# Kernel tuning notes

Hardware: AMD Instinct MI355X
Metric: run time of the kernel (lower is better)

The kernel has to match this reference:

```python
import jax, jax.numpy as jnp
import numpy as np

N, T, F_IN, E, H, FW = 4096, 64, 8, 256, 512, 32
LN_EPS = 1e-5


def setup_inputs() -> dict:
    key = jax.random.key(0)
    ks = jax.random.split(key, 16)
    nrm = lambda k, s, sc=0.05: jax.random.normal(k, s, dtype=jnp.float32) * sc
    return {
        "x": nrm(ks[0], (N, T, F_IN), 1.0),
        "We": nrm(ks[1], (E, F_IN)), "be": nrm(ks[2], (E,)),
        "Wih0": nrm(ks[3], (4 * H, E)), "Whh0": nrm(ks[4], (4 * H, H)),
        "bih0": nrm(ks[5], (4 * H,)), "bhh0": nrm(ks[6], (4 * H,)),
        "Wih1": nrm(ks[7], (4 * H, H)), "Whh1": nrm(ks[8], (4 * H, H)),
        "bih1": nrm(ks[9], (4 * H,)), "bhh1": nrm(ks[10], (4 * H,)),
        "fc1_w": nrm(ks[11], (H, H)), "fc1_b": nrm(ks[12], (H,)),
        "ln_g": jnp.ones((H,), jnp.float32), "ln_b": jnp.zeros((H,), jnp.float32),
        "fc2_w": nrm(ks[13], (F_IN, H)), "fc2_b": nrm(ks[14], (F_IN,)),
    }


def _cell(x, h, c, Wih, Whh, bih, bhh):
    # PyTorch LSTM gate order: i, f, g, o
    g = x @ Wih.T + h @ Whh.T + (bih + bhh)
    i, f, gg, o = jnp.split(g, 4, axis=-1)
    c = jax.nn.sigmoid(f) * c + jax.nn.sigmoid(i) * jnp.tanh(gg)
    h = jax.nn.sigmoid(o) * jnp.tanh(c)
    return h, c


def _layer(xs, Wih, Whh, bih, bhh):
    # xs: (T, N, D) -> ys: (T, N, H), final (h, c)
    n = xs.shape[1]
    Hd = Whh.shape[1]
    h0 = jnp.zeros((n, Hd), xs.dtype)
    def step(carry, x_t):
        h, c = carry
        h, c = _cell(x_t, h, c, Wih, Whh, bih, bhh)
        return (h, c), h
    (h, c), ys = jax.lax.scan(step, (h0, h0), xs)
    return ys, h, c


def reference(x, We, be, Wih0, Whh0, bih0, bhh0, Wih1, Whh1, bih1, bhh1,
              fc1_w, fc1_b, ln_g, ln_b, fc2_w, fc2_b):
    x_enc = x[:, :-1, :]          # (N, T-1, F)
    x0 = x[:, -1, :]              # (N, F)

    # ---- encoder ----
    emb = x_enc @ We.T + be       # (N, T-1, E)
    xs = jnp.swapaxes(emb, 0, 1)  # (T-1, N, E)
    ys0, h0e, c0e = _layer(xs, Wih0, Whh0, bih0, bhh0)
    _, h1e, c1e = _layer(ys0, Wih1, Whh1, bih1, bhh1)

    # ---- decoder head: Linear -> LayerNorm -> ReLU -> Linear ----
    def fc(h):
        z = h @ fc1_w.T + fc1_b
        mu = z.mean(-1, keepdims=True)
        var = z.var(-1, keepdims=True)
        z = (z - mu) * jax.lax.rsqrt(var + LN_EPS) * ln_g + ln_b
        z = jax.nn.relu(z)
        return z @ fc2_w.T + fc2_b

    def dec_step(carry, _):
        xt, h0, c0, h1, c1 = carry
        e = xt @ We.T + be
        h0, c0 = _cell(e, h0, c0, Wih0, Whh0, bih0, bhh0)
        h1, c1 = _cell(h0, h1, c1, Wih1, Whh1, bih1, bhh1)
        y = fc(h1)
        return (y, h0, c0, h1, c1), y

    _, ys = jax.lax.scan(dec_step, (x0, h0e, c0e, h1e, c1e), None, length=FW)
    return jnp.swapaxes(ys, 0, 1)  # (N, FW, F)
```

## Files before the change

### kernel.cpp

```cpp
#include <hip/hip_runtime.h>
#include <math.h>

#define NB   4096
#define HID  512
#define G4H  2048
#define EDIM 256
#define FINP 8
#define TSTEPS 64
#define FWIN 32

typedef __bf16 bf16;
typedef bf16  bf16x8 __attribute__((ext_vector_type(8)));
typedef float f32x4  __attribute__((ext_vector_type(4)));

__device__ __forceinline__ float sigf(float x) { return 1.0f / (1.0f + __expf(-x)); }
__device__ __forceinline__ float tanhf_(float x) { return 2.0f * sigf(2.0f * x) - 1.0f; }

__device__ __forceinline__ void gload16(const void* g, void* l) {
    __builtin_amdgcn_global_load_lds((const __attribute__((address_space(1))) void*)g,
                                     (__attribute__((address_space(3))) void*)l, 16, 0, 0);
}

__device__ __forceinline__ void gemm_pass(
    const bf16* __restrict__ A, int lda,
    const bf16* __restrict__ W, int ldw,
    int m0, int n0,
    bf16* As, bf16* Ws,
    f32x4 (&acc)[4][4])
{
    const int tid  = threadIdx.x;
    const int lane = tid & 63;
    const int w    = tid >> 6;
    const int wr   = w >> 1, wc = w & 1;
    const int koct = lane >> 4;
    const int l16  = lane & 15;

    const int lin0 = tid;
    const int lin1 = tid + 256;
    const int ar0 = lin0 >> 2, ac0 = (lin0 & 3) * 8;
    const int ar1 = lin1 >> 2, ac1 = (lin1 & 3) * 8;

    for (int k0 = 0; k0 < HID; k0 += 32) {
        __syncthreads();
        gload16(A + (size_t)(m0 + ar0) * lda + k0 + ac0, As + lin0 * 8);
        gload16(A + (size_t)(m0 + ar1) * lda + k0 + ac1, As + lin1 * 8);
        gload16(W + (size_t)(n0 + ar0) * ldw + k0 + ac0, Ws + lin0 * 8);
        gload16(W + (size_t)(n0 + ar1) * ldw + k0 + ac1, Ws + lin1 * 8);
        __syncthreads();
        bf16x8 af[4], bfr[4];
#pragma unroll
        for (int m = 0; m < 4; ++m)
            af[m] = *(const bf16x8*)&As[(wr * 64 + m * 16 + l16) * 32 + koct * 8];
#pragma unroll
        for (int n = 0; n < 4; ++n)
            bfr[n] = *(const bf16x8*)&Ws[(wc * 64 + n * 16 + l16) * 32 + koct * 8];
#pragma unroll
        for (int m = 0; m < 4; ++m)
#pragma unroll
            for (int n = 0; n < 4; ++n)
                acc[m][n] = __builtin_amdgcn_mfma_f32_16x16x32_bf16(af[m], bfr[n], acc[m][n], 0, 0, 0);
    }
}

template<int NPASS, bool HASX>
__global__ __launch_bounds__(256)
void lstm_mfma(const bf16* __restrict__ A1, const bf16* __restrict__ W1,
               const bf16* __restrict__ A2, const bf16* __restrict__ W2,
               const float* __restrict__ Wfc, const float* __restrict__ bias,
               const float* __restrict__ xA, int sx,
               float* __restrict__ cst, bf16* __restrict__ hdst)
{
    __shared__ bf16 As[128 * 32];
    __shared__ bf16 Ws[128 * 32];
    f32x4 acc[4][4];
#pragma unroll
    for (int m = 0; m < 4; ++m)
#pragma unroll
        for (int n = 0; n < 4; ++n)
            acc[m][n] = (f32x4){0.f, 0.f, 0.f, 0.f};

    const int m0 = blockIdx.x * 128, n0 = blockIdx.y * 128;
    gemm_pass(A1, 1024, W1, 512, m0, n0, As, Ws, acc);
    if constexpr (NPASS == 2)
        gemm_pass(A2, 1024, W2, 512, m0, n0, As, Ws, acc);

    const int tid = threadIdx.x, lane = tid & 63, w = tid >> 6;
    const int wr = w >> 1, wc = w & 1, l16 = lane & 15, lq = lane >> 4;
    const int hu = blockIdx.y * 32 + wc * 16 + l16;
    const int jb = n0 + wc * 64 + l16;

    float bq[4];
    float wf[4][8];
#pragma unroll
    for (int g = 0; g < 4; ++g) {
        bq[g] = bias[jb + g * 16];
        if constexpr (HASX) {
            const float* wrow = Wfc + (size_t)(jb + g * 16) * 8;
            f32x4 w0 = *(const f32x4*)wrow;
            f32x4 w1 = *(const f32x4*)(wrow + 4);
#pragma unroll
            for (int e = 0; e < 4; ++e) { wf[g][e] = w0[e]; wf[g][e + 4] = w1[e]; }
        }
    }

#pragma unroll
    for (int m = 0; m < 4; ++m) {
        const int rb = m0 + wr * 64 + m * 16 + lq * 4;
#pragma unroll
        for (int q = 0; q < 4; ++q) {
            const int r = rb + q;
            float d0 = 0.f, d1 = 0.f, d2 = 0.f, d3 = 0.f;
            if constexpr (HASX) {
                const float* xr = xA + (size_t)r * sx;
#pragma unroll
                for (int e = 0; e < 8; ++e) {
                    float xv = xr[e];
                    d0 += xv * wf[0][e]; d1 += xv * wf[1][e];
                    d2 += xv * wf[2][e]; d3 += xv * wf[3][e];
                }
            }
            float gi = acc[m][0][q] + bq[0] + d0;
            float gf = acc[m][1][q] + bq[1] + d1;
            float gg = acc[m][2][q] + bq[2] + d2;
            float go = acc[m][3][q] + bq[3] + d3;
            float iv = sigf(gi), fv = sigf(gf), gv = tanhf_(gg), ov = sigf(go);
            size_t ci = (size_t)r * HID + hu;
            float cn = fv * cst[ci] + iv * gv;
            cst[ci] = cn;
            hdst[(size_t)r * 1024 + hu] = (bf16)(ov * tanhf_(cn));
        }
    }
}

__global__ __launch_bounds__(256)
void fc1_mfma(const bf16* __restrict__ A, const bf16* __restrict__ W,
              const float* __restrict__ bias, float* __restrict__ Z)
{
    __shared__ bf16 As[128 * 32];
    __shared__ bf16 Ws[128 * 32];
    f32x4 acc[4][4];
#pragma unroll
    for (int m = 0; m < 4; ++m)
#pragma unroll
        for (int n = 0; n < 4; ++n)
            acc[m][n] = (f32x4){0.f, 0.f, 0.f, 0.f};

    const int m0 = blockIdx.x * 128, n0 = blockIdx.y * 128;
    gemm_pass(A, 1024, W, 512, m0, n0, As, Ws, acc);

    const int tid = threadIdx.x, lane = tid & 63, w = tid >> 6;
    const int wr = w >> 1, wc = w & 1, l16 = lane & 15, lq = lane >> 4;
#pragma unroll
    for (int m = 0; m < 4; ++m) {
        const int rb = m0 + wr * 64 + m * 16 + lq * 4;
#pragma unroll
        for (int n = 0; n < 4; ++n) {
            const int col = n0 + wc * 64 + n * 16 + l16;
            float bv = bias[col];
#pragma unroll
            for (int q = 0; q < 4; ++q)
                Z[(size_t)(rb + q) * HID + col] = acc[m][n][q] + bv;
        }
    }
}

__global__ __launch_bounds__(256)
void ln_fc2_kernel(const float* __restrict__ Z, const float* __restrict__ lng,
                   const float* __restrict__ lnb, const float* __restrict__ w2,
                   const float* __restrict__ b2, float* __restrict__ out)
{
    int wave = threadIdx.x >> 6;
    int lane = threadIdx.x & 63;
    int n = blockIdx.x * 4 + wave;
    const float* zr = Z + (size_t)n * HID;

    float v[8];
    float s1 = 0.f, s2 = 0.f;
#pragma unroll
    for (int j = 0; j < 8; ++j) {
        v[j] = zr[lane + j * 64];
        s1 += v[j];
        s2 += v[j] * v[j];
    }
#pragma unroll
    for (int off = 32; off; off >>= 1) {
        s1 += __shfl_down(s1, off);
        s2 += __shfl_down(s2, off);
    }
    s1 = __shfl(s1, 0);
    s2 = __shfl(s2, 0);
    float mu = s1 * (1.f / 512.f);
    float var = s2 * (1.f / 512.f) - mu * mu;
    float rs = rsqrtf(var + 1e-5f);

    float y[8];
#pragma unroll
    for (int f = 0; f < 8; ++f) y[f] = 0.f;
#pragma unroll
    for (int j = 0; j < 8; ++j) {
        int h = lane + j * 64;
        float zn = (v[j] - mu) * rs * lng[h] + lnb[h];
        zn = fmaxf(zn, 0.f);
#pragma unroll
        for (int f = 0; f < 8; ++f) y[f] += zn * w2[f * HID + h];
    }
#pragma unroll
    for (int f = 0; f < 8; ++f)
#pragma unroll
        for (int off = 32; off; off >>= 1) y[f] += __shfl_down(y[f], off);

    if (lane == 0) {
#pragma unroll
        for (int f = 0; f < 8; ++f) out[(size_t)n * 256 + f] = y[f] + b2[f];
    }
}

__device__ __forceinline__ int remap_j(int j) {
    int gate = j >> 9, hu = j & 511;
    return ((hu >> 4) << 6) + (gate << 4) + (hu & 15);
}

__global__ void fold_small(const float* __restrict__ Wih0, const float* __restrict__ We,
                           const float* __restrict__ be, const float* __restrict__ bih0,
                           const float* __restrict__ bhh0, const float* __restrict__ bih1,
                           const float* __restrict__ bhh1,
                           float* __restrict__ Wf0c, float* __restrict__ bf0c,
                           float* __restrict__ bs1c)
{
    int j = blockIdx.x * 256 + threadIdx.x;
    if (j >= G4H) return;
    int jn = remap_j(j);
    float acc[FINP];
#pragma unroll
    for (int f = 0; f < FINP; ++f) acc[f] = 0.f;
    float bacc = 0.f;
    for (int e = 0; e < EDIM; ++e) {
        float wv = Wih0[(size_t)j * EDIM + e];
        bacc += wv * be[e];
#pragma unroll
        for (int f = 0; f < FINP; ++f) acc[f] += wv * We[e * FINP + f];
    }
#pragma unroll
    for (int f = 0; f < FINP; ++f) Wf0c[(size_t)jn * FINP + f] = acc[f];
    bf0c[jn] = bacc + bih0[j] + bhh0[j];
    bs1c[jn] = bih1[j] + bhh1[j];
}

__global__ void conv_w(const float* __restrict__ W0, const float* __restrict__ W1,
                       const float* __restrict__ W2,
                       bf16* __restrict__ O0, bf16* __restrict__ O1, bf16* __restrict__ O2)
{
    int j = blockIdx.x;
    int which = blockIdx.y;
    const float* src = which == 0 ? W0 : which == 1 ? W1 : W2;
    bf16* dst = which == 0 ? O0 : which == 1 ? O1 : O2;
    int jn = remap_j(j);
    for (int k = threadIdx.x; k < HID; k += 256)
        dst[(size_t)jn * HID + k] = (bf16)src[(size_t)j * HID + k];
}

__global__ void conv_fc1(const float* __restrict__ W, bf16* __restrict__ O)
{
    int j = blockIdx.x;
    for (int k = threadIdx.x; k < HID; k += 256)
        O[(size_t)j * HID + k] = (bf16)W[(size_t)j * HID + k];
}

extern "C" void kernel_launch(void* const* d_in, const int* in_sizes, int n_in,
                              void* d_out, int out_size, void* d_ws, size_t ws_size,
                              hipStream_t stream)
{
    const float* x    = (const float*)d_in[0];
    const float* We   = (const float*)d_in[1];
    const float* be   = (const float*)d_in[2];
    const float* Wih0 = (const float*)d_in[3];
    const float* Whh0 = (const float*)d_in[4];
    const float* bih0 = (const float*)d_in[5];
    const float* bhh0 = (const float*)d_in[6];
    const float* Wih1 = (const float*)d_in[7];
    const float* Whh1 = (const float*)d_in[8];
    const float* bih1 = (const float*)d_in[9];
    const float* bhh1 = (const float*)d_in[10];
    const float* fc1w = (const float*)d_in[11];
    const float* fc1b = (const float*)d_in[12];
    const float* lng  = (const float*)d_in[13];
    const float* lnb  = (const float*)d_in[14];
    const float* fc2w = (const float*)d_in[15];
    const float* fc2b = (const float*)d_in[16];
    float* out = (float*)d_out;

    char* p = (char*)d_ws;
    auto alloc = [&](size_t bytes) -> void* {
        void* r = (void*)p;
        p += (bytes + 255) & ~(size_t)255;
        return r;
    };
    bf16*  Whh0c = (bf16*)alloc((size_t)G4H * HID * 2);
    bf16*  Wih1c = (bf16*)alloc((size_t)G4H * HID * 2);
    bf16*  Whh1c = (bf16*)alloc((size_t)G4H * HID * 2);
    bf16*  fc1wb = (bf16*)alloc((size_t)HID * HID * 2);
    float* Wf0c  = (float*)alloc((size_t)G4H * FINP * 4);
    float* bf0c  = (float*)alloc((size_t)G4H * 4);
    float* bs1c  = (float*)alloc((size_t)G4H * 4);
    const size_t SLAB = (size_t)NB * 1024;
    bf16*  AB1   = (bf16*)alloc(2 * SLAB * 2);
    float* c0    = (float*)alloc((size_t)NB * HID * 4);
    float* c1    = (float*)alloc((size_t)NB * HID * 4);
    float* Z     = (float*)alloc((size_t)NB * HID * 4);

    hipMemsetAsync(AB1, 0, SLAB * 2, stream);
    hipMemsetAsync(c0, 0, (size_t)NB * HID * 4, stream);
    hipMemsetAsync(c1, 0, (size_t)NB * HID * 4, stream);

    fold_small<<<8, 256, 0, stream>>>(Wih0, We, be, bih0, bhh0, bih1, bhh1, Wf0c, bf0c, bs1c);
    conv_w<<<dim3(G4H, 3), 256, 0, stream>>>(Whh0, Wih1, Whh1, Whh0c, Wih1c, Whh1c);
    conv_fc1<<<HID, 256, 0, stream>>>(fc1w, fc1wb);

    dim3 lg(32, 16), lb(256);
    int pp = 0;

    for (int t = 0; t < TSTEPS - 1; ++t) {
        bf16* Pp = AB1 + (size_t)pp * SLAB;
        bf16* Pq = AB1 + (size_t)(pp ^ 1) * SLAB;
        lstm_mfma<1, true><<<lg, lb, 0, stream>>>(Pp, Whh0c, nullptr, nullptr,
                                                  Wf0c, bf0c, x + (size_t)t * FINP, TSTEPS * FINP,
                                                  c0, Pq);
        lstm_mfma<2, false><<<lg, lb, 0, stream>>>(Pq, Wih1c, Pp + 512, Whh1c,
                                                   nullptr, bs1c, nullptr, 0,
                                                   c1, Pq + 512);
        pp ^= 1;
    }

    for (int s = 0; s < FWIN; ++s) {
        bf16* Pp = AB1 + (size_t)pp * SLAB;
        bf16* Pq = AB1 + (size_t)(pp ^ 1) * SLAB;
        const float* xA = (s == 0) ? (x + (size_t)(TSTEPS - 1) * FINP)
                                   : (out + (size_t)(s - 1) * FINP);
        int sx = (s == 0) ? (TSTEPS * FINP) : (FWIN * FINP);
        lstm_mfma<1, true><<<lg, lb, 0, stream>>>(Pp, Whh0c, nullptr, nullptr,
                                                  Wf0c, bf0c, xA, sx, c0, Pq);
        lstm_mfma<2, false><<<lg, lb, 0, stream>>>(Pq, Wih1c, Pp + 512, Whh1c,
                                                   nullptr, bs1c, nullptr, 0,
                                                   c1, Pq + 512);
        fc1_mfma<<<dim3(32, 4), lb, 0, stream>>>(Pq + 512, fc1wb, fc1b, Z);
        ln_fc2_kernel<<<NB / 4, 256, 0, stream>>>(Z, lng, lnb, fc2w, fc2b, out + (size_t)s * FINP);
        pp ^= 1;
    }
}
```

Baseline: 5.442 ms.

## Wavefront-fuse encoder LSTM layers, double-buffer GEMM K loop, swizzle workgroups

The encoder now runs layer 0 at step t+1 and layer 1 at step t in one kernel, halving the number of recurrent launches and doubling the grid per launch. The first layer-0 step, whose inputs are all zero, is replaced by an elementwise init kernel. The GEMM K loop is double-buffered in LDS so the next tile loads while the current one computes, workgroup IDs are swizzled for cache locality, and h0/h1 move into separate compact buffers. The cost is more complex buffer indexing and twice the LDS per block, which can lower occupancy.

```diff
diff --git a/kernel.cpp b/kernel.cpp
--- a/kernel.cpp
+++ b/kernel.cpp
@@ -21,12 +21,18 @@
                                      (__attribute__((address_space(3))) void*)l, 16, 0, 0);
 }
 
-__device__ __forceinline__ void gemm_pass(
-    const bf16* __restrict__ A, int lda,
-    const bf16* __restrict__ W, int ldw,
-    int m0, int n0,
-    bf16* As, bf16* Ws,
-    f32x4 (&acc)[4][4])
+__device__ __forceinline__ void swz32(int& bx, int& by) {
+    int nwg  = (int)(gridDim.x * gridDim.y);
+    int orig = (int)(blockIdx.x + blockIdx.y * gridDim.x);
+    int swz  = (orig & 7) * (nwg >> 3) + (orig >> 3);
+    bx = swz & 31;
+    by = swz >> 5;
+}
+
+__device__ __forceinline__ void gemm_acc(
+    const bf16* __restrict__ A1, const bf16* __restrict__ W1,
+    const bf16* __restrict__ A2, const bf16* __restrict__ W2, int npass,
+    int m0, int n0, bf16 (&As)[2][4096], bf16 (&Ws)[2][4096], f32x4 (&acc)[4][4])
 {
     const int tid  = threadIdx.x;
     const int lane = tid & 63;
@@ -34,75 +40,65 @@
     const int wr   = w >> 1, wc = w & 1;
     const int koct = lane >> 4;
     const int l16  = lane & 15;
-
-    const int lin0 = tid;
-    const int lin1 = tid + 256;
+    const int lin0 = tid, lin1 = tid + 256;
     const int ar0 = lin0 >> 2, ac0 = (lin0 & 3) * 8;
     const int ar1 = lin1 >> 2, ac1 = (lin1 & 3) * 8;
-
-    for (int k0 = 0; k0 < HID; k0 += 32) {
-        __syncthreads();
-        gload16(A + (size_t)(m0 + ar0) * lda + k0 + ac0, As + lin0 * 8);
-        gload16(A + (size_t)(m0 + ar1) * lda + k0 + ac1, As + lin1 * 8);
-        gload16(W + (size_t)(n0 + ar0) * ldw + k0 + ac0, Ws + lin0 * 8);
-        gload16(W + (size_t)(n0 + ar1) * ldw + k0 + ac1, Ws + lin1 * 8);
-        __syncthreads();
+    const int NK = npass << 4;
+
+    auto stage = [&](int s, int b) {
+        const bf16* A = (s < 16) ? A1 : A2;
+        const bf16* W = (s < 16) ? W1 : W2;
+        const int k0 = (s & 15) << 5;
+        gload16(A + (size_t)(m0 + ar0) * HID + k0 + ac0, &As[b][lin0 * 8]);
+        gload16(A + (size_t)(m0 + ar1) * HID + k0 + ac1, &As[b][lin1 * 8]);
+        gload16(W + (size_t)(n0 + ar0) * HID + k0 + ac0, &Ws[b][lin0 * 8]);
+        gload16(W + (size_t)(n0 + ar1) * HID + k0 + ac1, &Ws[b][lin1 * 8]);
+    };
+
+    stage(0, 0);
+    __syncthreads();
+    int cur = 0;
+    for (int s = 0; s < NK; ++s) {
+        if (s + 1 < NK) stage(s + 1, cur ^ 1);
         bf16x8 af[4], bfr[4];
 #pragma unroll
         for (int m = 0; m < 4; ++m)
-            af[m] = *(const bf16x8*)&As[(wr * 64 + m * 16 + l16) * 32 + koct * 8];
+            af[m] = *(const bf16x8*)&As[cur][(wr * 64 + m * 16 + l16) * 32 + koct * 8];
 #pragma unroll
         for (int n = 0; n < 4; ++n)
-            bfr[n] = *(const bf16x8*)&Ws[(wc * 64 + n * 16 + l16) * 32 + koct * 8];
+            bfr[n] = *(const bf16x8*)&Ws[cur][(wc * 64 + n * 16 + l16) * 32 + koct * 8];
 #pragma unroll
         for (int m = 0; m < 4; ++m)
 #pragma unroll
             for (int n = 0; n < 4; ++n)
                 acc[m][n] = __builtin_amdgcn_mfma_f32_16x16x32_bf16(af[m], bfr[n], acc[m][n], 0, 0, 0);
-    }
-}
-
-template<int NPASS, bool HASX>
-__global__ __launch_bounds__(256)
-void lstm_mfma(const bf16* __restrict__ A1, const bf16* __restrict__ W1,
-               const bf16* __restrict__ A2, const bf16* __restrict__ W2,
-               const float* __restrict__ Wfc, const float* __restrict__ bias,
-               const float* __restrict__ xA, int sx,
-               float* __restrict__ cst, bf16* __restrict__ hdst)
-{
-    __shared__ bf16 As[128 * 32];
-    __shared__ bf16 Ws[128 * 32];
-    f32x4 acc[4][4];
-#pragma unroll
-    for (int m = 0; m < 4; ++m)
-#pragma unroll
-        for (int n = 0; n < 4; ++n)
-            acc[m][n] = (f32x4){0.f, 0.f, 0.f, 0.f};
-
-    const int m0 = blockIdx.x * 128, n0 = blockIdx.y * 128;
-    gemm_pass(A1, 1024, W1, 512, m0, n0, As, Ws, acc);
-    if constexpr (NPASS == 2)
-        gemm_pass(A2, 1024, W2, 512, m0, n0, As, Ws, acc);
-
+        __syncthreads();
+        cur ^= 1;
+    }
+}
+
+template<bool HASX>
+__device__ __forceinline__ void lstm_epi(f32x4 (&acc)[4][4],
+    const float* __restrict__ Wfc, const float* __restrict__ bias,
+    const float* __restrict__ xA, int sx,
+    float* __restrict__ cst, bf16* __restrict__ hdst, int m0, int n0)
+{
     const int tid = threadIdx.x, lane = tid & 63, w = tid >> 6;
     const int wr = w >> 1, wc = w & 1, l16 = lane & 15, lq = lane >> 4;
-    const int hu = blockIdx.y * 32 + wc * 16 + l16;
+    const int hu = (n0 >> 2) + wc * 16 + l16;
     const int jb = n0 + wc * 64 + l16;
 
     float bq[4];
-    float wf[4][8];
+    f32x4 wf0[4], wf1[4];
 #pragma unroll
     for (int g = 0; g < 4; ++g) {
         bq[g] = bias[jb + g * 16];
         if constexpr (HASX) {
             const float* wrow = Wfc + (size_t)(jb + g * 16) * 8;
-            f32x4 w0 = *(const f32x4*)wrow;
-            f32x4 w1 = *(const f32x4*)(wrow + 4);
-#pragma unroll
-            for (int e = 0; e < 4; ++e) { wf[g][e] = w0[e]; wf[g][e + 4] = w1[e]; }
+            wf0[g] = *(const f32x4*)wrow;
+            wf1[g] = *(const f32x4*)(wrow + 4);
         }
     }
-
 #pragma unroll
     for (int m = 0; m < 4; ++m) {
         const int rb = m0 + wr * 64 + m * 16 + lq * 4;
@@ -112,12 +108,16 @@
             float d0 = 0.f, d1 = 0.f, d2 = 0.f, d3 = 0.f;
             if constexpr (HASX) {
                 const float* xr = xA + (size_t)r * sx;
-#pragma unroll
-                for (int e = 0; e < 8; ++e) {
-                    float xv = xr[e];
-                    d0 += xv * wf[0][e]; d1 += xv * wf[1][e];
-                    d2 += xv * wf[2][e]; d3 += xv * wf[3][e];
-                }
+                f32x4 xv0 = *(const f32x4*)xr;
+                f32x4 xv1 = *(const f32x4*)(xr + 4);
+                f32x4 p0 = xv0 * wf0[0] + xv1 * wf1[0];
+                f32x4 p1 = xv0 * wf0[1] + xv1 * wf1[1];
+                f32x4 p2 = xv0 * wf0[2] + xv1 * wf1[2];
+                f32x4 p3 = xv0 * wf0[3] + xv1 * wf1[3];
+                d0 = p0[0] + p0[1] + p0[2] + p0[3];
+                d1 = p1[0] + p1[1] + p1[2] + p1[3];
+                d2 = p2[0] + p2[1] + p2[2] + p2[3];
+                d3 = p3[0] + p3[1] + p3[2] + p3[3];
             }
             float gi = acc[m][0][q] + bq[0] + d0;
             float gf = acc[m][1][q] + bq[1] + d1;
@@ -127,26 +127,99 @@
             size_t ci = (size_t)r * HID + hu;
             float cn = fv * cst[ci] + iv * gv;
             cst[ci] = cn;
-            hdst[(size_t)r * 1024 + hu] = (bf16)(ov * tanhf_(cn));
+            hdst[ci] = (bf16)(ov * tanhf_(cn));
         }
     }
+}
+
+template<int NPASS, bool HASX>
+__global__ __launch_bounds__(256)
+void lstm_step(const bf16* __restrict__ A1, const bf16* __restrict__ W1,
+               const bf16* __restrict__ A2, const bf16* __restrict__ W2,
+               const float* __restrict__ Wfc, const float* __restrict__ bias,
+               const float* __restrict__ xA, int sx,
+               float* __restrict__ cst, bf16* __restrict__ hdst)
+{
+    __shared__ bf16 As[2][4096], Ws[2][4096];
+    int bx, by; swz32(bx, by);
+    const int m0 = bx * 128, n0 = by * 128;
+    f32x4 acc[4][4];
+#pragma unroll
+    for (int m = 0; m < 4; ++m)
+#pragma unroll
+        for (int n = 0; n < 4; ++n) acc[m][n] = (f32x4){0.f, 0.f, 0.f, 0.f};
+    gemm_acc(A1, W1, A2, W2, NPASS, m0, n0, As, Ws, acc);
+    lstm_epi<HASX>(acc, Wfc, bias, xA, sx, cst, hdst, m0, n0);
+}
+
+template<bool L1TWO>
+__global__ __launch_bounds__(256)
+void enc_fused(const bf16* __restrict__ h0_in, const bf16* __restrict__ Whh0c,
+               const float* __restrict__ Wf0c, const float* __restrict__ bf0c,
+               const float* __restrict__ xA,
+               bf16* __restrict__ h0_out, float* __restrict__ c0,
+               const bf16* __restrict__ Wih1c, const bf16* __restrict__ h1_in,
+               const bf16* __restrict__ Whh1c, const float* __restrict__ bs1c,
+               bf16* __restrict__ h1_out, float* __restrict__ c1)
+{
+    __shared__ bf16 As[2][4096], Ws[2][4096];
+    int bx, by; swz32(bx, by);
+    const int m0 = bx * 128;
+    f32x4 acc[4][4];
+#pragma unroll
+    for (int m = 0; m < 4; ++m)
+#pragma unroll
+        for (int n = 0; n < 4; ++n) acc[m][n] = (f32x4){0.f, 0.f, 0.f, 0.f};
+    if (by < 16) {
+        const int n0 = by * 128;
+        gemm_acc(h0_in, Whh0c, nullptr, nullptr, 1, m0, n0, As, Ws, acc);
+        lstm_epi<true>(acc, Wf0c, bf0c, xA, TSTEPS * FINP, c0, h0_out, m0, n0);
+    } else {
+        const int n0 = (by - 16) * 128;
+        gemm_acc(h0_in, Wih1c, h1_in, Whh1c, L1TWO ? 2 : 1, m0, n0, As, Ws, acc);
+        lstm_epi<false>(acc, nullptr, bs1c, nullptr, 0, c1, h1_out, m0, n0);
+    }
+}
+
+__global__ __launch_bounds__(256)
+void init_step(const float* __restrict__ x, const float* __restrict__ Wf0c,
+               const float* __restrict__ bf0c, bf16* __restrict__ h0,
+               float* __restrict__ c0)
+{
+    int idx = blockIdx.x * 256 + threadIdx.x;
+    int r = idx >> 9, hu = idx & 511;
+    const float* xr = x + (size_t)r * (TSTEPS * FINP);
+    f32x4 xv0 = *(const f32x4*)xr;
+    f32x4 xv1 = *(const f32x4*)(xr + 4);
+    int jb = ((hu >> 4) << 6) + (hu & 15);
+    float g[4];
+#pragma unroll
+    for (int gg = 0; gg < 4; ++gg) {
+        const float* wrow = Wf0c + (size_t)(jb + gg * 16) * 8;
+        f32x4 w0 = *(const f32x4*)wrow;
+        f32x4 w1 = *(const f32x4*)(wrow + 4);
+        f32x4 p = xv0 * w0 + xv1 * w1;
+        g[gg] = bf0c[jb + gg * 16] + p[0] + p[1] + p[2] + p[3];
+    }
+    float iv = sigf(g[0]), gv = tanhf_(g[2]), ov = sigf(g[3]);
+    float cn = iv * gv;
+    c0[idx] = cn;
+    h0[idx] = (bf16)(ov * tanhf_(cn));
 }
 
 __global__ __launch_bounds__(256)
 void fc1_mfma(const bf16* __restrict__ A, const bf16* __restrict__ W,
               const float* __restrict__ bias, float* __restrict__ Z)
 {
-    __shared__ bf16 As[128 * 32];
-    __shared__ bf16 Ws[128 * 32];
+    __shared__ bf16 As[2][4096], Ws[2][4096];
+    int bx, by; swz32(bx, by);
+    const int m0 = bx * 128, n0 = by * 128;
     f32x4 acc[4][4];
 #pragma unroll
     for (int m = 0; m < 4; ++m)
 #pragma unroll
-        for (int n = 0; n < 4; ++n)
-            acc[m][n] = (f32x4){0.f, 0.f, 0.f, 0.f};
-
-    const int m0 = blockIdx.x * 128, n0 = blockIdx.y * 128;
-    gemm_pass(A, 1024, W, 512, m0, n0, As, Ws, acc);
+        for (int n = 0; n < 4; ++n) acc[m][n] = (f32x4){0.f, 0.f, 0.f, 0.f};
+    gemm_acc(A, W, nullptr, nullptr, 1, m0, n0, As, Ws, acc);
 
     const int tid = threadIdx.x, lane = tid & 63, w = tid >> 6;
     const int wr = w >> 1, wc = w & 1, l16 = lane & 15, lq = lane >> 4;
@@ -302,48 +375,46 @@
     float* Wf0c  = (float*)alloc((size_t)G4H * FINP * 4);
     float* bf0c  = (float*)alloc((size_t)G4H * 4);
     float* bs1c  = (float*)alloc((size_t)G4H * 4);
-    const size_t SLAB = (size_t)NB * 1024;
-    bf16*  AB1   = (bf16*)alloc(2 * SLAB * 2);
-    float* c0    = (float*)alloc((size_t)NB * HID * 4);
-    float* c1    = (float*)alloc((size_t)NB * HID * 4);
-    float* Z     = (float*)alloc((size_t)NB * HID * 4);
-
-    hipMemsetAsync(AB1, 0, SLAB * 2, stream);
-    hipMemsetAsync(c0, 0, (size_t)NB * HID * 4, stream);
-    hipMemsetAsync(c1, 0, (size_t)NB * HID * 4, stream);
+    const size_t S = (size_t)NB * HID;
+    bf16*  H0[2]; H0[0] = (bf16*)alloc(S * 2); H0[1] = (bf16*)alloc(S * 2);
+    bf16*  H1[2]; H1[0] = (bf16*)alloc(S * 2); H1[1] = (bf16*)alloc(S * 2);
+    float* c0    = (float*)alloc(S * 4);
+    float* c1    = (float*)alloc(S * 4);
+    float* Z     = (float*)alloc(S * 4);
+
+    hipMemsetAsync(c1, 0, S * 4, stream);
 
     fold_small<<<8, 256, 0, stream>>>(Wih0, We, be, bih0, bhh0, bih1, bhh1, Wf0c, bf0c, bs1c);
     conv_w<<<dim3(G4H, 3), 256, 0, stream>>>(Whh0, Wih1, Whh1, Whh0c, Wih1c, Whh1c);
     conv_fc1<<<HID, 256, 0, stream>>>(fc1w, fc1wb);
 
-    dim3 lg(32, 16), lb(256);
-    int pp = 0;
-
-    for (int t = 0; t < TSTEPS - 1; ++t) {
-        bf16* Pp = AB1 + (size_t)pp * SLAB;
-        bf16* Pq = AB1 + (size_t)(pp ^ 1) * SLAB;
-        lstm_mfma<1, true><<<lg, lb, 0, stream>>>(Pp, Whh0c, nullptr, nullptr,
-                                                  Wf0c, bf0c, x + (size_t)t * FINP, TSTEPS * FINP,
-                                                  c0, Pq);
-        lstm_mfma<2, false><<<lg, lb, 0, stream>>>(Pq, Wih1c, Pp + 512, Whh1c,
-                                                   nullptr, bs1c, nullptr, 0,
-                                                   c1, Pq + 512);
-        pp ^= 1;
-    }
+    init_step<<<NB * HID / 256, 256, 0, stream>>>(x, Wf0c, bf0c, H0[0], c0);
+
+    dim3 fg(32, 32), lb(256);
+    for (int t = 0; t < TSTEPS - 2; ++t) {
+        if (t == 0)
+            enc_fused<false><<<fg, lb, 0, stream>>>(H0[0], Whh0c, Wf0c, bf0c,
+                x + (size_t)1 * FINP, H0[1], c0,
+                Wih1c, nullptr, Whh1c, bs1c, H1[0], c1);
+        else
+            enc_fused<true><<<fg, lb, 0, stream>>>(H0[t & 1], Whh0c, Wf0c, bf0c,
+                x + (size_t)(t + 1) * FINP, H0[(t + 1) & 1], c0,
+                Wih1c, H1[(t + 1) & 1], Whh1c, bs1c, H1[t & 1], c1);
+    }
+    lstm_step<2, false><<<dim3(32, 16), lb, 0, stream>>>(
+        H0[0], Wih1c, H1[1], Whh1c, nullptr, bs1c, nullptr, 0, c1, H1[0]);
 
     for (int s = 0; s < FWIN; ++s) {
-        bf16* Pp = AB1 + (size_t)pp * SLAB;
-        bf16* Pq = AB1 + (size_t)(pp ^ 1) * SLAB;
         const float* xA = (s == 0) ? (x + (size_t)(TSTEPS - 1) * FINP)
                                    : (out + (size_t)(s - 1) * FINP);
         int sx = (s == 0) ? (TSTEPS * FINP) : (FWIN * FINP);
-        lstm_mfma<1, true><<<lg, lb, 0, stream>>>(Pp, Whh0c, nullptr, nullptr,
-                                                  Wf0c, bf0c, xA, sx, c0, Pq);
-        lstm_mfma<2, false><<<lg, lb, 0, stream>>>(Pq, Wih1c, Pp + 512, Whh1c,
-                                                   nullptr, bs1c, nullptr, 0,
-                                                   c1, Pq + 512);
-        fc1_mfma<<<dim3(32, 4), lb, 0, stream>>>(Pq + 512, fc1wb, fc1b, Z);
-        ln_fc2_kernel<<<NB / 4, 256, 0, stream>>>(Z, lng, lnb, fc2w, fc2b, out + (size_t)s * FINP);
-        pp ^= 1;
-    }
-}
+        lstm_step<1, true><<<dim3(32, 16), lb, 0, stream>>>(
+            H0[s & 1], Whh0c, nullptr, nullptr, Wf0c, bf0c, xA, sx, c0, H0[(s + 1) & 1]);
+        lstm_step<2, false><<<dim3(32, 16), lb, 0, stream>>>(
+            H0[(s + 1) & 1], Wih1c, H1[s & 1], Whh1c, nullptr, bs1c, nullptr, 0,
+            c1, H1[(s + 1) & 1]);
+        fc1_mfma<<<dim3(32, 4), lb, 0, stream>>>(H1[(s + 1) & 1], fc1wb, fc1b, Z);
+        ln_fc2_kernel<<<NB / 4, 256, 0, stream>>>(Z, lng, lnb, fc2w, fc2b,
+                                                  out + (size_t)s * FINP);
+    }
+}
```

Result: slower. 6.196 ms (+13.9%).
